# Optimization experiments

Hardware: AMD Instinct MI355X
Metric: run time of the kernel (lower is better)

## Reference

```python
import jax, jax.numpy as jnp
import numpy as np

DIM = 2048
NUM_LADDERS = 3
DEPTH = 5
EPS = 0.01


def setup_inputs() -> dict:
    key = jax.random.key(0)
    ks = jax.random.split(key, 5)
    s = 1.0 / np.sqrt(DIM)
    x = jax.random.normal(ks[0], (4, 2048, DIM), dtype=jnp.float32)
    U_w = jax.random.uniform(ks[1], (DIM, DIM), jnp.float32, -s, s)          # U.weight  [out,in]
    gate_w = jax.random.uniform(ks[2], (DIM, DIM), jnp.float32, -s, s)       # gate_proj.weight
    ladder_w = jax.random.uniform(ks[3], (NUM_LADDERS, DEPTH + 1, DIM), jnp.float32, -s, s)
    V_w = jax.random.uniform(ks[4], (DIM, NUM_LADDERS), jnp.float32, -1.0 / np.sqrt(NUM_LADDERS), 1.0 / np.sqrt(NUM_LADDERS))
    return {"x": x, "U_w": U_w, "gate_w": gate_w, "ladder_w": ladder_w, "V_w": V_w}


def _continued_fraction(a_cf, eps):
    # a_cf: (..., depth). Evaluate a_1/(1 + a_2/(1 + ... a_d/1)) with
    # epsilon-guarded denominators (pole avoidance).
    d = a_cf.shape[-1]
    f = jnp.zeros(a_cf.shape[:-1], a_cf.dtype)
    for k in reversed(range(d)):  # tiny fixed depth: loop is fine
        denom = 1.0 + f
        denom = jnp.where(jnp.abs(denom) < eps,
                          jnp.where(denom >= 0, eps, -eps), denom)
        f = a_cf[..., k] / denom
    return f


def reference(x, U_w, gate_w, ladder_w, V_w):
    linear_out = jnp.einsum('bsd,od->bso', x, U_w)                 # U(x)
    gated_x = jax.nn.sigmoid(jnp.einsum('bsd,od->bso', x, gate_w)) * x
    # All ladders at once: (b,s,L,depth+1)
    a = jnp.einsum('bsd,lkd->bslk', gated_x, ladder_w)
    a0 = a[..., 0]                                                 # (b,s,L)
    z = a0 + _continued_fraction(a[..., 1:], EPS)                  # (b,s,L)
    combined = jnp.einsum('bsl,dl->bsd', z, V_w)                   # V(z)
    return linear_out + combined
```

## Files before the change

kernel.cpp:

```cpp
#include <hip/hip_runtime.h>
#include <cstdint>
#include <cstddef>

#define DIM 2048
#define NROWS 8192
#define NL 3
#define DEPTH 5
#define CF_EPS 0.01f

typedef __attribute__((ext_vector_type(8))) __bf16 bfrag;
typedef __attribute__((ext_vector_type(4))) float f32x4;

typedef __attribute__((address_space(1))) void gvoid;
typedef __attribute__((address_space(3))) void lvoid;

__device__ __forceinline__ void gld_lds16(const void* g, void* l) {
    __builtin_amdgcn_global_load_lds((gvoid*)g, (lvoid*)l, 16, 0, 0);
}

template<bool SPLIT>
__global__ __launch_bounds__(256) void mfma_gemm(
    const ushort* __restrict__ Ah, const ushort* __restrict__ Al,
    const ushort* __restrict__ Bh, const ushort* __restrict__ Bl,
    float* __restrict__ C)
{
    constexpr int BK = 32;
    __shared__ __align__(16) ushort sAh[128 * BK];
    __shared__ __align__(16) ushort sBh[128 * BK];
    __shared__ __align__(16) ushort sAl[SPLIT ? 128 * BK : 8];
    __shared__ __align__(16) ushort sBl[SPLIT ? 128 * BK : 8];

    const int tid  = threadIdx.x;
    const int wave = tid >> 6;
    const int lane = tid & 63;
    const int wm   = wave & 1;
    const int wn   = wave >> 1;
    const int m0   = blockIdx.y * 128;
    const int n0   = blockIdx.x * 128;

    const size_t soff = (size_t)(wave * 32 + (lane >> 2)) * DIM + (lane & 3) * 8;
    const ushort* gA  = Ah + (size_t)m0 * DIM + soff;
    const ushort* gB  = Bh + (size_t)n0 * DIM + soff;
    const ushort* gAl = Al + (size_t)m0 * DIM + soff;
    const ushort* gBl = Bl + (size_t)n0 * DIM + soff;

    ushort* lA0 = &sAh[(wave * 32) * BK];
    ushort* lA1 = &sAh[(wave * 32 + 16) * BK];
    ushort* lB0 = &sBh[(wave * 32) * BK];
    ushort* lB1 = &sBh[(wave * 32 + 16) * BK];
    ushort* lAl0 = &sAl[SPLIT ? (wave * 32) * BK : 0];
    ushort* lAl1 = &sAl[SPLIT ? (wave * 32 + 16) * BK : 0];
    ushort* lBl0 = &sBl[SPLIT ? (wave * 32) * BK : 0];
    ushort* lBl1 = &sBl[SPLIT ? (wave * 32 + 16) * BK : 0];

    const int fm = lane & 15;
    const int fq = lane >> 4;

    f32x4 acc[4][4];
    #pragma unroll
    for (int i = 0; i < 4; ++i)
        #pragma unroll
        for (int j = 0; j < 4; ++j)
            acc[i][j] = (f32x4){0.f, 0.f, 0.f, 0.f};

    for (int k0 = 0; k0 < DIM; k0 += BK) {
        __syncthreads();
        gld_lds16(gA + k0, lA0);
        gld_lds16(gA + (size_t)16 * DIM + k0, lA1);
        gld_lds16(gB + k0, lB0);
        gld_lds16(gB + (size_t)16 * DIM + k0, lB1);
        if constexpr (SPLIT) {
            gld_lds16(gAl + k0, lAl0);
            gld_lds16(gAl + (size_t)16 * DIM + k0, lAl1);
            gld_lds16(gBl + k0, lBl0);
            gld_lds16(gBl + (size_t)16 * DIM + k0, lBl1);
        }
        __syncthreads();

        bfrag ah[4], bh[4], al[4], bl[4];
        #pragma unroll
        for (int i = 0; i < 4; ++i) {
            ah[i] = *(const bfrag*)&sAh[(wm * 64 + i * 16 + fm) * BK + fq * 8];
            bh[i] = *(const bfrag*)&sBh[(wn * 64 + i * 16 + fm) * BK + fq * 8];
            if constexpr (SPLIT) {
                al[i] = *(const bfrag*)&sAl[(wm * 64 + i * 16 + fm) * BK + fq * 8];
                bl[i] = *(const bfrag*)&sBl[(wn * 64 + i * 16 + fm) * BK + fq * 8];
            }
        }
        #pragma unroll
        for (int i = 0; i < 4; ++i)
            #pragma unroll
            for (int j = 0; j < 4; ++j) {
                acc[i][j] = __builtin_amdgcn_mfma_f32_16x16x32_bf16(ah[i], bh[j], acc[i][j], 0, 0, 0);
                if constexpr (SPLIT) {
                    acc[i][j] = __builtin_amdgcn_mfma_f32_16x16x32_bf16(ah[i], bl[j], acc[i][j], 0, 0, 0);
                    acc[i][j] = __builtin_amdgcn_mfma_f32_16x16x32_bf16(al[i], bh[j], acc[i][j], 0, 0, 0);
                }
            }
    }

    #pragma unroll
    for (int i = 0; i < 4; ++i) {
        const int rowb = m0 + wm * 64 + i * 16 + fq * 4;
        #pragma unroll
        for (int j = 0; j < 4; ++j) {
            const int col = n0 + wn * 64 + j * 16 + fm;
            #pragma unroll
            for (int r = 0; r < 4; ++r)
                C[(size_t)(rowb + r) * DIM + col] = acc[i][j][r];
        }
    }
}

__device__ __forceinline__ ushort f2bf_bits(float f) {
    __bf16 h = (__bf16)f;
    return __builtin_bit_cast(unsigned short, h);
}
__device__ __forceinline__ float bfbits2f(ushort u) {
    __bf16 h = __builtin_bit_cast(__bf16, u);
    return (float)h;
}

union U16x8 { ushort u[8]; uint4 v; };

__global__ __launch_bounds__(256) void split2(const float* __restrict__ src,
                                              ushort* __restrict__ hi,
                                              ushort* __restrict__ lo)
{
    const size_t i0 = ((size_t)blockIdx.x * 256 + threadIdx.x) * 8;
    const float4 v0 = *(const float4*)(src + i0);
    const float4 v1 = *(const float4*)(src + i0 + 4);
    const float f[8] = {v0.x, v0.y, v0.z, v0.w, v1.x, v1.y, v1.z, v1.w};
    U16x8 h, l;
    #pragma unroll
    for (int j = 0; j < 8; ++j) {
        const ushort hb = f2bf_bits(f[j]);
        h.u[j] = hb;
        l.u[j] = f2bf_bits(f[j] - bfbits2f(hb));
    }
    *(uint4*)(hi + i0) = h.v;
    *(uint4*)(lo + i0) = l.v;
}

__global__ __launch_bounds__(256) void tobf16(const float* __restrict__ src,
                                              ushort* __restrict__ dst)
{
    const size_t i0 = ((size_t)blockIdx.x * 256 + threadIdx.x) * 8;
    const float4 v0 = *(const float4*)(src + i0);
    const float4 v1 = *(const float4*)(src + i0 + 4);
    const float f[8] = {v0.x, v0.y, v0.z, v0.w, v1.x, v1.y, v1.z, v1.w};
    U16x8 h;
    #pragma unroll
    for (int j = 0; j < 8; ++j) h.u[j] = f2bf_bits(f[j]);
    *(uint4*)(dst + i0) = h.v;
}

#define BMF 128
#define BNF 128
#define BKF 16
#define LDAF 132

__global__ __launch_bounds__(256) void sgemm_dual(
    const float* __restrict__ X,
    const float* __restrict__ Uw,
    const float* __restrict__ Gw,
    float* __restrict__ outLin,
    float* __restrict__ outGate)
{
    __shared__ float As[BKF][LDAF];
    __shared__ float Bs[BKF][LDAF];

    const int tid = threadIdx.x;
    const int n0 = blockIdx.x * BNF;
    const int m0 = blockIdx.y * BMF;
    const bool isGate = (n0 >= DIM);
    const float* W = isGate ? Gw : Uw;
    float* C = isGate ? outGate : outLin;
    const int nb = isGate ? (n0 - DIM) : n0;

    const int lr = tid >> 2;
    const int lc = (tid & 3) << 2;

    const float* pa0 = X + (size_t)(m0 + lr) * DIM + lc;
    const float* pa1 = X + (size_t)(m0 + lr + 64) * DIM + lc;
    const float* pb0 = W + (size_t)(nb + lr) * DIM + lc;
    const float* pb1 = W + (size_t)(nb + lr + 64) * DIM + lc;

    const int tx = tid & 15;
    const int ty = tid >> 4;

    float acc[8][8];
    #pragma unroll
    for (int i = 0; i < 8; ++i)
        #pragma unroll
        for (int j = 0; j < 8; ++j) acc[i][j] = 0.f;

    for (int k0 = 0; k0 < DIM; k0 += BKF) {
        const float4 a0 = *(const float4*)(pa0 + k0);
        const float4 a1 = *(const float4*)(pa1 + k0);
        const float4 b0 = *(const float4*)(pb0 + k0);
        const float4 b1 = *(const float4*)(pb1 + k0);
        __syncthreads();
        As[lc + 0][lr] = a0.x; As[lc + 1][lr] = a0.y; As[lc + 2][lr] = a0.z; As[lc + 3][lr] = a0.w;
        As[lc + 0][lr + 64] = a1.x; As[lc + 1][lr + 64] = a1.y; As[lc + 2][lr + 64] = a1.z; As[lc + 3][lr + 64] = a1.w;
        Bs[lc + 0][lr] = b0.x; Bs[lc + 1][lr] = b0.y; Bs[lc + 2][lr] = b0.z; Bs[lc + 3][lr] = b0.w;
        Bs[lc + 0][lr + 64] = b1.x; Bs[lc + 1][lr + 64] = b1.y; Bs[lc + 2][lr + 64] = b1.z; Bs[lc + 3][lr + 64] = b1.w;
        __syncthreads();
        #pragma unroll
        for (int kk = 0; kk < BKF; ++kk) {
            float av[8], bv[8];
            *(float4*)&av[0] = *(const float4*)&As[kk][ty * 8];
            *(float4*)&av[4] = *(const float4*)&As[kk][ty * 8 + 4];
            *(float4*)&bv[0] = *(const float4*)&Bs[kk][tx * 8];
            *(float4*)&bv[4] = *(const float4*)&Bs[kk][tx * 8 + 4];
            #pragma unroll
            for (int i = 0; i < 8; ++i)
                #pragma unroll
                for (int j = 0; j < 8; ++j)
                    acc[i][j] = fmaf(av[i], bv[j], acc[i][j]);
        }
    }

    #pragma unroll
    for (int i = 0; i < 8; ++i) {
        float* crow = C + (size_t)(m0 + ty * 8 + i) * DIM + nb + tx * 8;
        *(float4*)crow       = make_float4(acc[i][0], acc[i][1], acc[i][2], acc[i][3]);
        *(float4*)(crow + 4) = make_float4(acc[i][4], acc[i][5], acc[i][6], acc[i][7]);
    }
}

__global__ __launch_bounds__(256) void ladder_epilogue(
    const float* __restrict__ X,
    const float* __restrict__ G,
    const float* __restrict__ Lw,
    const float* __restrict__ Vw,
    float* __restrict__ Out)
{
    const int r = blockIdx.x;
    const int tid = threadIdx.x;
    const int d0 = tid * 8;
    const float* xrow = X + (size_t)r * DIM;
    const float* grow = G + (size_t)r * DIM;

    const float4 xv0 = *(const float4*)(xrow + d0);
    const float4 xv1 = *(const float4*)(xrow + d0 + 4);
    const float4 gv0 = *(const float4*)(grow + d0);
    const float4 gv1 = *(const float4*)(grow + d0 + 4);

    float gated[8];
    {
        const float gx[8] = {gv0.x, gv0.y, gv0.z, gv0.w, gv1.x, gv1.y, gv1.z, gv1.w};
        const float xx[8] = {xv0.x, xv0.y, xv0.z, xv0.w, xv1.x, xv1.y, xv1.z, xv1.w};
        #pragma unroll
        for (int j = 0; j < 8; ++j) {
            const float s = 1.0f / (1.0f + __expf(-gx[j]));
            gated[j] = s * xx[j];
        }
    }

    float part[NL * (DEPTH + 1)];
    #pragma unroll
    for (int lk = 0; lk < NL * (DEPTH + 1); ++lk) {
        const float* lrow = Lw + (size_t)lk * DIM + d0;
        const float4 w0 = *(const float4*)lrow;
        const float4 w1 = *(const float4*)(lrow + 4);
        part[lk] = gated[0] * w0.x + gated[1] * w0.y + gated[2] * w0.z + gated[3] * w0.w
                 + gated[4] * w1.x + gated[5] * w1.y + gated[6] * w1.z + gated[7] * w1.w;
    }

    #pragma unroll
    for (int off = 32; off > 0; off >>= 1) {
        #pragma unroll
        for (int lk = 0; lk < NL * (DEPTH + 1); ++lk)
            part[lk] += __shfl_down(part[lk], off, 64);
    }

    __shared__ float red[4][NL * (DEPTH + 1)];
    __shared__ float zsh[NL];
    const int wave = tid >> 6;
    const int lane = tid & 63;
    if (lane == 0) {
        #pragma unroll
        for (int lk = 0; lk < NL * (DEPTH + 1); ++lk) red[wave][lk] = part[lk];
    }
    __syncthreads();
    if (tid < NL) {
        float a[DEPTH + 1];
        #pragma unroll
        for (int k = 0; k < DEPTH + 1; ++k)
            a[k] = red[0][tid * 6 + k] + red[1][tid * 6 + k]
                 + red[2][tid * 6 + k] + red[3][tid * 6 + k];
        float f = 0.f;
        #pragma unroll
        for (int k = DEPTH - 1; k >= 0; --k) {
            float denom = 1.f + f;
            if (fabsf(denom) < CF_EPS) denom = (denom >= 0.f) ? CF_EPS : -CF_EPS;
            f = a[k + 1] / denom;
        }
        zsh[tid] = a[0] + f;
    }
    __syncthreads();
    const float z0 = zsh[0], z1 = zsh[1], z2 = zsh[2];

    float* orow = Out + (size_t)r * DIM + d0;
    const float4 o0 = *(const float4*)orow;
    const float4 o1 = *(const float4*)(orow + 4);
    float ov[8] = {o0.x, o0.y, o0.z, o0.w, o1.x, o1.y, o1.z, o1.w};
    #pragma unroll
    for (int j = 0; j < 8; ++j) {
        const float* vp = Vw + (size_t)(d0 + j) * NL;
        ov[j] += z0 * vp[0] + z1 * vp[1] + z2 * vp[2];
    }
    *(float4*)orow       = make_float4(ov[0], ov[1], ov[2], ov[3]);
    *(float4*)(orow + 4) = make_float4(ov[4], ov[5], ov[6], ov[7]);
}

extern "C" void kernel_launch(void* const* d_in, const int* in_sizes, int n_in,
                              void* d_out, int out_size, void* d_ws, size_t ws_size,
                              hipStream_t stream) {
    const float* X  = (const float*)d_in[0];
    const float* Uw = (const float*)d_in[1];
    const float* Gw = (const float*)d_in[2];
    const float* Lw = (const float*)d_in[3];
    const float* Vw = (const float*)d_in[4];
    float* out = (float*)d_out;

    const size_t WS_NEED = 159383552ull;
    char* ws = (char*)d_ws;
    float* gbuf = (float*)ws;

    if (ws_size >= WS_NEED) {
        ushort* Xh  = (ushort*)(ws + 67108864);
        ushort* Xl  = (ushort*)(ws + 100663296);
        ushort* Gwh = (ushort*)(ws + 134217728);
        ushort* Gwl = (ushort*)(ws + 142606336);
        ushort* Uwh = (ushort*)(ws + 150994944);

        split2<<<dim3(8192), dim3(256), 0, stream>>>(X, Xh, Xl);
        split2<<<dim3(2048), dim3(256), 0, stream>>>(Gw, Gwh, Gwl);
        tobf16<<<dim3(2048), dim3(256), 0, stream>>>(Uw, Uwh);

        dim3 grid(DIM / 128, NROWS / 128);
        mfma_gemm<false><<<grid, dim3(256), 0, stream>>>(Xh, Xh, Uwh, Uwh, out);
        mfma_gemm<true ><<<grid, dim3(256), 0, stream>>>(Xh, Xl, Gwh, Gwl, gbuf);
    } else {
        dim3 grid(2 * DIM / BNF, NROWS / BMF);
        sgemm_dual<<<grid, dim3(256), 0, stream>>>(X, Uw, Gw, out, gbuf);
    }
    ladder_epilogue<<<dim3(NROWS), dim3(256), 0, stream>>>(X, gbuf, Lw, Vw, out);
}
```

Before: 574.2 us.

## Fuse U and gate MFMA GEMMs into one kernel sharing the X tile

```diff
diff --git a/kernel.cpp b/kernel.cpp
--- a/kernel.cpp
+++ b/kernel.cpp
@@ -18,17 +18,19 @@
     __builtin_amdgcn_global_load_lds((gvoid*)g, (lvoid*)l, 16, 0, 0);
 }
 
-template<bool SPLIT>
-__global__ __launch_bounds__(256) void mfma_gemm(
-    const ushort* __restrict__ Ah, const ushort* __restrict__ Al,
-    const ushort* __restrict__ Bh, const ushort* __restrict__ Bl,
-    float* __restrict__ C)
+__global__ __launch_bounds__(256) void fused_mfma(
+    const ushort* __restrict__ Xh, const ushort* __restrict__ Xl,
+    const ushort* __restrict__ Gwh, const ushort* __restrict__ Gwl,
+    const ushort* __restrict__ Uwh,
+    const float* __restrict__ X,
+    float* __restrict__ outU, float* __restrict__ gated)
 {
     constexpr int BK = 32;
     __shared__ __align__(16) ushort sAh[128 * BK];
+    __shared__ __align__(16) ushort sAl[128 * BK];
     __shared__ __align__(16) ushort sBh[128 * BK];
-    __shared__ __align__(16) ushort sAl[SPLIT ? 128 * BK : 8];
-    __shared__ __align__(16) ushort sBl[SPLIT ? 128 * BK : 8];
+    __shared__ __align__(16) ushort sBl[128 * BK];
+    __shared__ __align__(16) ushort sUh[128 * BK];
 
     const int tid  = threadIdx.x;
     const int wave = tid >> 6;
@@ -39,64 +41,60 @@
     const int n0   = blockIdx.x * 128;
 
     const size_t soff = (size_t)(wave * 32 + (lane >> 2)) * DIM + (lane & 3) * 8;
-    const ushort* gA  = Ah + (size_t)m0 * DIM + soff;
-    const ushort* gB  = Bh + (size_t)n0 * DIM + soff;
-    const ushort* gAl = Al + (size_t)m0 * DIM + soff;
-    const ushort* gBl = Bl + (size_t)n0 * DIM + soff;
-
-    ushort* lA0 = &sAh[(wave * 32) * BK];
-    ushort* lA1 = &sAh[(wave * 32 + 16) * BK];
-    ushort* lB0 = &sBh[(wave * 32) * BK];
-    ushort* lB1 = &sBh[(wave * 32 + 16) * BK];
-    ushort* lAl0 = &sAl[SPLIT ? (wave * 32) * BK : 0];
-    ushort* lAl1 = &sAl[SPLIT ? (wave * 32 + 16) * BK : 0];
-    ushort* lBl0 = &sBl[SPLIT ? (wave * 32) * BK : 0];
-    ushort* lBl1 = &sBl[SPLIT ? (wave * 32 + 16) * BK : 0];
+    const ushort* gAh = Xh  + (size_t)m0 * DIM + soff;
+    const ushort* gAl = Xl  + (size_t)m0 * DIM + soff;
+    const ushort* gBh = Gwh + (size_t)n0 * DIM + soff;
+    const ushort* gBl = Gwl + (size_t)n0 * DIM + soff;
+    const ushort* gUh = Uwh + (size_t)n0 * DIM + soff;
+
+    ushort* lAh0 = &sAh[(wave * 32) * BK];  ushort* lAh1 = &sAh[(wave * 32 + 16) * BK];
+    ushort* lAl0 = &sAl[(wave * 32) * BK];  ushort* lAl1 = &sAl[(wave * 32 + 16) * BK];
+    ushort* lBh0 = &sBh[(wave * 32) * BK];  ushort* lBh1 = &sBh[(wave * 32 + 16) * BK];
+    ushort* lBl0 = &sBl[(wave * 32) * BK];  ushort* lBl1 = &sBl[(wave * 32 + 16) * BK];
+    ushort* lUh0 = &sUh[(wave * 32) * BK];  ushort* lUh1 = &sUh[(wave * 32 + 16) * BK];
 
     const int fm = lane & 15;
     const int fq = lane >> 4;
 
-    f32x4 acc[4][4];
+    f32x4 uacc[4][4], gacc[4][4];
     #pragma unroll
     for (int i = 0; i < 4; ++i)
         #pragma unroll
-        for (int j = 0; j < 4; ++j)
-            acc[i][j] = (f32x4){0.f, 0.f, 0.f, 0.f};
+        for (int j = 0; j < 4; ++j) {
+            uacc[i][j] = (f32x4){0.f, 0.f, 0.f, 0.f};
+            gacc[i][j] = (f32x4){0.f, 0.f, 0.f, 0.f};
+        }
 
     for (int k0 = 0; k0 < DIM; k0 += BK) {
         __syncthreads();
-        gld_lds16(gA + k0, lA0);
-        gld_lds16(gA + (size_t)16 * DIM + k0, lA1);
-        gld_lds16(gB + k0, lB0);
-        gld_lds16(gB + (size_t)16 * DIM + k0, lB1);
-        if constexpr (SPLIT) {
-            gld_lds16(gAl + k0, lAl0);
-            gld_lds16(gAl + (size_t)16 * DIM + k0, lAl1);
-            gld_lds16(gBl + k0, lBl0);
-            gld_lds16(gBl + (size_t)16 * DIM + k0, lBl1);
-        }
+        gld_lds16(gAh + k0, lAh0);  gld_lds16(gAh + (size_t)16 * DIM + k0, lAh1);
+        gld_lds16(gAl + k0, lAl0);  gld_lds16(gAl + (size_t)16 * DIM + k0, lAl1);
+        gld_lds16(gBh + k0, lBh0);  gld_lds16(gBh + (size_t)16 * DIM + k0, lBh1);
+        gld_lds16(gBl + k0, lBl0);  gld_lds16(gBl + (size_t)16 * DIM + k0, lBl1);
+        gld_lds16(gUh + k0, lUh0);  gld_lds16(gUh + (size_t)16 * DIM + k0, lUh1);
         __syncthreads();
 
-        bfrag ah[4], bh[4], al[4], bl[4];
+        bfrag bh[4], bl[4], uh[4];
+        #pragma unroll
+        for (int j = 0; j < 4; ++j) {
+            const int bo = (wn * 64 + j * 16 + fm) * BK + fq * 8;
+            bh[j] = *(const bfrag*)&sBh[bo];
+            bl[j] = *(const bfrag*)&sBl[bo];
+            uh[j] = *(const bfrag*)&sUh[bo];
+        }
         #pragma unroll
         for (int i = 0; i < 4; ++i) {
-            ah[i] = *(const bfrag*)&sAh[(wm * 64 + i * 16 + fm) * BK + fq * 8];
-            bh[i] = *(const bfrag*)&sBh[(wn * 64 + i * 16 + fm) * BK + fq * 8];
-            if constexpr (SPLIT) {
-                al[i] = *(const bfrag*)&sAl[(wm * 64 + i * 16 + fm) * BK + fq * 8];
-                bl[i] = *(const bfrag*)&sBl[(wn * 64 + i * 16 + fm) * BK + fq * 8];
-            }
-        }
-        #pragma unroll
-        for (int i = 0; i < 4; ++i)
+            const int ao = (wm * 64 + i * 16 + fm) * BK + fq * 8;
+            const bfrag ah = *(const bfrag*)&sAh[ao];
+            const bfrag al = *(const bfrag*)&sAl[ao];
             #pragma unroll
             for (int j = 0; j < 4; ++j) {
-                acc[i][j] = __builtin_amdgcn_mfma_f32_16x16x32_bf16(ah[i], bh[j], acc[i][j], 0, 0, 0);
-                if constexpr (SPLIT) {
-                    acc[i][j] = __builtin_amdgcn_mfma_f32_16x16x32_bf16(ah[i], bl[j], acc[i][j], 0, 0, 0);
-                    acc[i][j] = __builtin_amdgcn_mfma_f32_16x16x32_bf16(al[i], bh[j], acc[i][j], 0, 0, 0);
-                }
+                uacc[i][j] = __builtin_amdgcn_mfma_f32_16x16x32_bf16(ah, uh[j], uacc[i][j], 0, 0, 0);
+                gacc[i][j] = __builtin_amdgcn_mfma_f32_16x16x32_bf16(ah, bh[j], gacc[i][j], 0, 0, 0);
+                gacc[i][j] = __builtin_amdgcn_mfma_f32_16x16x32_bf16(ah, bl[j], gacc[i][j], 0, 0, 0);
+                gacc[i][j] = __builtin_amdgcn_mfma_f32_16x16x32_bf16(al, bh[j], gacc[i][j], 0, 0, 0);
             }
+        }
     }
 
     #pragma unroll
@@ -106,8 +104,12 @@
         for (int j = 0; j < 4; ++j) {
             const int col = n0 + wn * 64 + j * 16 + fm;
             #pragma unroll
-            for (int r = 0; r < 4; ++r)
-                C[(size_t)(rowb + r) * DIM + col] = acc[i][j][r];
+            for (int r = 0; r < 4; ++r) {
+                const size_t idx = (size_t)(rowb + r) * DIM + col;
+                outU[idx] = uacc[i][j][r];
+                const float s = 1.0f / (1.0f + __expf(-gacc[i][j][r]));
+                gated[idx] = s * X[idx];
+            }
         }
     }
 }
@@ -155,83 +157,8 @@
     *(uint4*)(dst + i0) = h.v;
 }
 
-#define BMF 128
-#define BNF 128
-#define BKF 16
-#define LDAF 132
-
-__global__ __launch_bounds__(256) void sgemm_dual(
-    const float* __restrict__ X,
-    const float* __restrict__ Uw,
-    const float* __restrict__ Gw,
-    float* __restrict__ outLin,
-    float* __restrict__ outGate)
-{
-    __shared__ float As[BKF][LDAF];
-    __shared__ float Bs[BKF][LDAF];
-
-    const int tid = threadIdx.x;
-    const int n0 = blockIdx.x * BNF;
-    const int m0 = blockIdx.y * BMF;
-    const bool isGate = (n0 >= DIM);
-    const float* W = isGate ? Gw : Uw;
-    float* C = isGate ? outGate : outLin;
-    const int nb = isGate ? (n0 - DIM) : n0;
-
-    const int lr = tid >> 2;
-    const int lc = (tid & 3) << 2;
-
-    const float* pa0 = X + (size_t)(m0 + lr) * DIM + lc;
-    const float* pa1 = X + (size_t)(m0 + lr + 64) * DIM + lc;
-    const float* pb0 = W + (size_t)(nb + lr) * DIM + lc;
-    const float* pb1 = W + (size_t)(nb + lr + 64) * DIM + lc;
-
-    const int tx = tid & 15;
-    const int ty = tid >> 4;
-
-    float acc[8][8];
-    #pragma unroll
-    for (int i = 0; i < 8; ++i)
-        #pragma unroll
-        for (int j = 0; j < 8; ++j) acc[i][j] = 0.f;
-
-    for (int k0 = 0; k0 < DIM; k0 += BKF) {
-        const float4 a0 = *(const float4*)(pa0 + k0);
-        const float4 a1 = *(const float4*)(pa1 + k0);
-        const float4 b0 = *(const float4*)(pb0 + k0);
-        const float4 b1 = *(const float4*)(pb1 + k0);
-        __syncthreads();
-        As[lc + 0][lr] = a0.x; As[lc + 1][lr] = a0.y; As[lc + 2][lr] = a0.z; As[lc + 3][lr] = a0.w;
-        As[lc + 0][lr + 64] = a1.x; As[lc + 1][lr + 64] = a1.y; As[lc + 2][lr + 64] = a1.z; As[lc + 3][lr + 64] = a1.w;
-        Bs[lc + 0][lr] = b0.x; Bs[lc + 1][lr] = b0.y; Bs[lc + 2][lr] = b0.z; Bs[lc + 3][lr] = b0.w;
-        Bs[lc + 0][lr + 64] = b1.x; Bs[lc + 1][lr + 64] = b1.y; Bs[lc + 2][lr + 64] = b1.z; Bs[lc + 3][lr + 64] = b1.w;
-        __syncthreads();
-        #pragma unroll
-        for (int kk = 0; kk < BKF; ++kk) {
-            float av[8], bv[8];
-            *(float4*)&av[0] = *(const float4*)&As[kk][ty * 8];
-            *(float4*)&av[4] = *(const float4*)&As[kk][ty * 8 + 4];
-            *(float4*)&bv[0] = *(const float4*)&Bs[kk][tx * 8];
-            *(float4*)&bv[4] = *(const float4*)&Bs[kk][tx * 8 + 4];
-            #pragma unroll
-            for (int i = 0; i < 8; ++i)
-                #pragma unroll
-                for (int j = 0; j < 8; ++j)
-                    acc[i][j] = fmaf(av[i], bv[j], acc[i][j]);
-        }
-    }
-
-    #pragma unroll
-    for (int i = 0; i < 8; ++i) {
-        float* crow = C + (size_t)(m0 + ty * 8 + i) * DIM + nb + tx * 8;
-        *(float4*)crow       = make_float4(acc[i][0], acc[i][1], acc[i][2], acc[i][3]);
-        *(float4*)(crow + 4) = make_float4(acc[i][4], acc[i][5], acc[i][6], acc[i][7]);
-    }
-}
-
 __global__ __launch_bounds__(256) void ladder_epilogue(
-    const float* __restrict__ X,
-    const float* __restrict__ G,
+    const float* __restrict__ Gt,
     const float* __restrict__ Lw,
     const float* __restrict__ Vw,
     float* __restrict__ Out)
@@ -239,24 +166,11 @@
     const int r = blockIdx.x;
     const int tid = threadIdx.x;
     const int d0 = tid * 8;
-    const float* xrow = X + (size_t)r * DIM;
-    const float* grow = G + (size_t)r * DIM;
-
-    const float4 xv0 = *(const float4*)(xrow + d0);
-    const float4 xv1 = *(const float4*)(xrow + d0 + 4);
-    const float4 gv0 = *(const float4*)(grow + d0);
-    const float4 gv1 = *(const float4*)(grow + d0 + 4);
-
-    float gated[8];
-    {
-        const float gx[8] = {gv0.x, gv0.y, gv0.z, gv0.w, gv1.x, gv1.y, gv1.z, gv1.w};
-        const float xx[8] = {xv0.x, xv0.y, xv0.z, xv0.w, xv1.x, xv1.y, xv1.z, xv1.w};
-        #pragma unroll
-        for (int j = 0; j < 8; ++j) {
-            const float s = 1.0f / (1.0f + __expf(-gx[j]));
-            gated[j] = s * xx[j];
-        }
-    }
+    const float* grow = Gt + (size_t)r * DIM;
+
+    const float4 g0 = *(const float4*)(grow + d0);
+    const float4 g1 = *(const float4*)(grow + d0 + 4);
+    const float gated[8] = {g0.x, g0.y, g0.z, g0.w, g1.x, g1.y, g1.z, g1.w};
 
     float part[NL * (DEPTH + 1)];
     #pragma unroll
@@ -325,27 +239,20 @@
     const float* Vw = (const float*)d_in[4];
     float* out = (float*)d_out;
 
-    const size_t WS_NEED = 159383552ull;
     char* ws = (char*)d_ws;
-    float* gbuf = (float*)ws;
-
-    if (ws_size >= WS_NEED) {
-        ushort* Xh  = (ushort*)(ws + 67108864);
-        ushort* Xl  = (ushort*)(ws + 100663296);
-        ushort* Gwh = (ushort*)(ws + 134217728);
-        ushort* Gwl = (ushort*)(ws + 142606336);
-        ushort* Uwh = (ushort*)(ws + 150994944);
-
-        split2<<<dim3(8192), dim3(256), 0, stream>>>(X, Xh, Xl);
-        split2<<<dim3(2048), dim3(256), 0, stream>>>(Gw, Gwh, Gwl);
-        tobf16<<<dim3(2048), dim3(256), 0, stream>>>(Uw, Uwh);
-
-        dim3 grid(DIM / 128, NROWS / 128);
-        mfma_gemm<false><<<grid, dim3(256), 0, stream>>>(Xh, Xh, Uwh, Uwh, out);
-        mfma_gemm<true ><<<grid, dim3(256), 0, stream>>>(Xh, Xl, Gwh, Gwl, gbuf);
-    } else {
-        dim3 grid(2 * DIM / BNF, NROWS / BMF);
-        sgemm_dual<<<grid, dim3(256), 0, stream>>>(X, Uw, Gw, out, gbuf);
-    }
-    ladder_epilogue<<<dim3(NROWS), dim3(256), 0, stream>>>(X, gbuf, Lw, Vw, out);
-}
+    float*  gated = (float*)ws;
+    ushort* Xh  = (ushort*)(ws + 67108864);
+    ushort* Xl  = (ushort*)(ws + 100663296);
+    ushort* Gwh = (ushort*)(ws + 134217728);
+    ushort* Gwl = (ushort*)(ws + 142606336);
+    ushort* Uwh = (ushort*)(ws + 150994944);
+
+    split2<<<dim3(8192), dim3(256), 0, stream>>>(X, Xh, Xl);
+    split2<<<dim3(2048), dim3(256), 0, stream>>>(Gw, Gwh, Gwl);
+    tobf16<<<dim3(2048), dim3(256), 0, stream>>>(Uw, Uwh);
+
+    dim3 grid(DIM / 128, NROWS / 128);
+    fused_mfma<<<grid, dim3(256), 0, stream>>>(Xh, Xl, Gwh, Gwl, Uwh, X, out, gated);
+
+    ladder_epilogue<<<dim3(NROWS), dim3(256), 0, stream>>>(gated, Lw, Vw, out);
+}
```

New measurement: 762.2 us. 1.33x slower.
